# Optimization experiments

Hardware: AMD Instinct MI355X
Metric: run time of the kernel (lower is better)

The kernel has to match this reference:

```python
import jax, jax.numpy as jnp
import numpy as np

B, T, H, E = 256, 512, 512, 32

def setup_inputs() -> dict:
    key = jax.random.key(0)
    ks = jax.random.split(key, 7)
    events = jax.random.randint(ks[0], (B, T), 0, E, dtype=jnp.int32)
    # strictly increasing event times (as produced by cumsum of positive gaps upstream)
    gaps = jax.random.uniform(ks[1], (B, T), dtype=jnp.float32) * 0.1 + 1e-3
    times = jnp.cumsum(gaps, axis=1)
    emb = jax.random.normal(ks[2], (E, H), dtype=jnp.float32) * 0.05
    # 5 gate Linears (input, forget, output, cell, decay) stacked: [2H, 5H]
    W_gates = jax.random.normal(ks[3], (2 * H, 5 * H), dtype=jnp.float32) * (1.0 / np.sqrt(2 * H))
    b_gates = jnp.zeros((5 * H,), dtype=jnp.float32)
    W_int = jax.random.normal(ks[4], (H, E), dtype=jnp.float32) * (1.0 / np.sqrt(H))
    b_int = jnp.zeros((E,), dtype=jnp.float32)
    return {"events": events, "times": times, "emb": emb,
            "W_gates": W_gates, "b_gates": b_gates, "W_int": W_int, "b_int": b_int}

def reference(events, times, emb, W_gates, b_gates, W_int, b_int):
    Bs, Ts = events.shape
    Hs = emb.shape[1]
    x_seq = emb[events]                                   # [B,T,H] embedding lookup
    deltas = jnp.concatenate([times[:, :1], jnp.diff(times, axis=1)], axis=1)  # [B,T]
    xs = (jnp.transpose(x_seq, (1, 0, 2)), deltas.T)      # ([T,B,H], [T,B])

    def step(carry, inp):
        h, c = carry
        x, dt = inp
        comb = jnp.concatenate([x, h], axis=1)            # [B,2H]
        g = comb @ W_gates + b_gates                      # [B,5H] fused gate GEMM
        i, f, o, c_tilde, d = jnp.split(g, 5, axis=1)
        i, f, o, c_tilde = jnp.tanh(i), jnp.tanh(f), jnp.tanh(o), jnp.tanh(c_tilde)
        decay = jax.nn.softplus(d)
        c_dec = c * jnp.exp(-decay * dt[:, None])
        c_n = f * c_dec + i * c_tilde
        h_n = o * jnp.tanh(c_n)
        lam = jax.nn.softplus(h_n @ W_int + b_int)        # [B,E]
        return (h_n, c_n), (lam, h_n)

    h0 = jnp.zeros((Bs, Hs), dtype=times.dtype)
    c0 = jnp.zeros((Bs, Hs), dtype=times.dtype)
    _, (lams, hs) = jax.lax.scan(step, (h0, c0), xs)
    intensities = jnp.transpose(lams, (1, 0, 2))          # [B,T,E]
    hidden_states = jnp.transpose(hs, (1, 0, 2))          # [B,T,H]
    return intensities, hidden_states
```

## Files before the change

kernel.cpp:

```cpp
#include <hip/hip_runtime.h>
#include <math.h>


#define Bb   256
#define Tt   512
#define Hh   512
#define Ee   32
#define G5H  2560
#define NTHR 256
#define RT   16
#define CT   32

typedef __attribute__((ext_vector_type(8))) short f16x8;
typedef __attribute__((ext_vector_type(4))) float f32x4;
typedef __attribute__((ext_vector_type(4))) unsigned u32x4;
typedef __attribute__((ext_vector_type(2))) unsigned u32x2;

__device__ __forceinline__ float softplusf(float x) {
    return fmaxf(x, 0.f) + __logf(1.f + __expf(-fabsf(x)));
}
__device__ __forceinline__ float fast_tanh(float x) {
    const float t = fminf(fmaxf(x, -15.f), 15.f);
    const float e = __expf(2.f * t);
    return (e - 1.f) / (e + 1.f);
}
__device__ __forceinline__ unsigned short f2h(float f) {
    _Float16 h = (_Float16)f;
    return *reinterpret_cast<unsigned short*>(&h);
}

__device__ __forceinline__ void load_tagged8(const unsigned* p, u32x4 (&d)[8]) {
    asm volatile(
        "global_load_dwordx4 %0, %8, off sc0 sc1\n\t"
        "global_load_dwordx4 %1, %8, off offset:16 sc0 sc1\n\t"
        "global_load_dwordx4 %2, %8, off offset:128 sc0 sc1\n\t"
        "global_load_dwordx4 %3, %8, off offset:144 sc0 sc1\n\t"
        "global_load_dwordx4 %4, %8, off offset:256 sc0 sc1\n\t"
        "global_load_dwordx4 %5, %8, off offset:272 sc0 sc1\n\t"
        "global_load_dwordx4 %6, %8, off offset:384 sc0 sc1\n\t"
        "global_load_dwordx4 %7, %8, off offset:400 sc0 sc1\n\t"
        "s_waitcnt vmcnt(0)"
        : "=&v"(d[0]), "=&v"(d[1]), "=&v"(d[2]), "=&v"(d[3]),
          "=&v"(d[4]), "=&v"(d[5]), "=&v"(d[6]), "=&v"(d[7])
        : "v"(p) : "memory");
}
__device__ __forceinline__ void store_tagged(unsigned* p, unsigned data, unsigned tag) {
    u32x2 v; v.x = data; v.y = tag;
    asm volatile("global_store_dwordx2 %0, %1, off sc0 sc1"
                 :: "v"(p), "v"(v) : "memory");
}

__global__ __launch_bounds__(NTHR, 1)
void nhp_scan(const int* __restrict__ events, const float* __restrict__ times,
              const float* __restrict__ emb, const float* __restrict__ Wg,
              const float* __restrict__ bg, float* __restrict__ out_hid,
              unsigned* __restrict__ hb) {
    __shared__ float red[2][4][10][16][18];
    __shared__ float gx[Ee][5][34];
    __shared__ int   ev_s[2][RT];
    __shared__ float dt_s[2][RT];

    const int tid  = threadIdx.x, bid = blockIdx.x;
    const int rt   = bid & 15;
    const int ct   = bid >> 4;
    const int r0   = rt * RT;
    const int lane = tid & 63;
    const int ks   = tid >> 6;
    const int frow = lane & 15, kgrp = lane >> 4;
    const int erow = tid >> 4;
    const int ecp  = (tid & 15) * 2;

    for (int u = tid; u < Ee * 5 * CT; u += NTHR) {
        const int e = u / 160, r = u - e * 160;
        const int g = r >> 5, hc = r & 31;
        const int gcol = g * Hh + ct * CT + hc;
        float acc = bg[gcol];
        const float* er = emb + (size_t)e * Hh;
        for (int k = 0; k < Hh; k += 4) {
            acc += er[k]     * Wg[(size_t)k       * G5H + gcol];
            acc += er[k + 1] * Wg[(size_t)(k + 1) * G5H + gcol];
            acc += er[k + 2] * Wg[(size_t)(k + 2) * G5H + gcol];
            acc += er[k + 3] * Wg[(size_t)(k + 3) * G5H + gcol];
        }
        gx[e][g][hc ^ ((e & 7) << 2)] = acc;
    }

    f16x8 Bf[10][4];
    #pragma unroll
    for (int n = 0; n < 10; ++n) {
        const int col = (n >> 1) * Hh + ct * CT + (n & 1) * 16 + frow;
        #pragma unroll
        for (int kk = 0; kk < 4; ++kk) {
            const int k0 = ks * 128 + kk * 32 + kgrp * 8;
            union { f16x8 v; unsigned u[4]; } tmp;
            #pragma unroll
            for (int r = 0; r < 4; ++r) {
                const float w0 = Wg[(size_t)(Hh + k0 + 2 * r)     * G5H + col];
                const float w1 = Wg[(size_t)(Hh + k0 + 2 * r + 1) * G5H + col];
                tmp.u[r] = (unsigned)f2h(w0) | ((unsigned)f2h(w1) << 16);
            }
            Bf[n][kk] = tmp.v;
        }
    }

    float cA = 0.f, cB = 0.f;
    __syncthreads();

    for (int p = 0; p < Tt; ++p) {
        const int par = p & 1;
        if (tid < RT) {
            const int b = r0 + tid;
            ev_s[par][tid] = events[b * Tt + p];
            const float tp = times[b * Tt + p];
            dt_s[par][tid] = (p == 0) ? tp : tp - times[b * Tt + p - 1];
        }

        if (p > 0) {
            const unsigned* base = hb + ((size_t)((p - 1) & 1) * Bb * 256
                                 + (size_t)(r0 + frow) * 256 + ks * 64 + kgrp * 4) * 2;
            const unsigned want = (unsigned)p;
            u32x4 d[8];
            int guard = 0;
            for (;;) {
                load_tagged8(base, d);
                int ok = 1;
                #pragma unroll
                for (int i = 0; i < 8; ++i)
                    ok &= (d[i].y == want) & (d[i].w == want);
                if (__all(ok)) break;
                if (++guard > 100000) break;
                __builtin_amdgcn_s_sleep(1);
            }
            f16x8 a[4];
            #pragma unroll
            for (int kk = 0; kk < 4; ++kk) {
                union { f16x8 v; unsigned u[4]; } t;
                t.u[0] = d[2 * kk].x;     t.u[1] = d[2 * kk].z;
                t.u[2] = d[2 * kk + 1].x; t.u[3] = d[2 * kk + 1].z;
                a[kk] = t.v;
            }
            f32x4 acc[10];
            #pragma unroll
            for (int n = 0; n < 10; ++n) acc[n] = (f32x4){0.f, 0.f, 0.f, 0.f};
            #pragma unroll
            for (int kk = 0; kk < 4; ++kk) {
                #pragma unroll
                for (int n = 0; n < 10; ++n)
                    acc[n] = __builtin_amdgcn_mfma_f32_16x16x32_f16(
                        a[kk], Bf[n][kk], acc[n], 0, 0, 0);
            }
            #pragma unroll
            for (int n = 0; n < 10; ++n)
                #pragma unroll
                for (int r = 0; r < 4; ++r)
                    red[par][ks][n][kgrp * 4 + r][frow] = acc[n][r];
        }
        __syncthreads();

        const int   e  = ev_s[par][erow];
        const float dt = dt_s[par][erow];
        const int   sc = (e & 7) << 2;
        float hn[2];
        {
            float v0[5], v1[5];
            const int tl0 = ecp >> 4, fc = ecp & 15;
            #pragma unroll
            for (int gt = 0; gt < 5; ++gt) {
                const float2 gv = *(const float2*)&gx[e][gt][ecp ^ sc];
                v0[gt] = gv.x; v1[gt] = gv.y;
                if (p > 0) {
                    const int tl = gt * 2 + tl0;
                    #pragma unroll
                    for (int s = 0; s < 4; ++s) {
                        const float2 pr = *(const float2*)&red[par][s][tl][erow][fc];
                        v0[gt] += pr.x; v1[gt] += pr.y;
                    }
                }
            }
            #pragma unroll
            for (int q = 0; q < 2; ++q) {
                const float* v = q ? v1 : v0;
                const float ig  = fast_tanh(v[0]);
                const float fg  = fast_tanh(v[1]);
                const float og  = fast_tanh(v[2]);
                const float ctl = fast_tanh(v[3]);
                const float dec = softplusf(v[4]);
                const float cpv = q ? cB : cA;
                const float cn  = fg * (cpv * __expf(-dec * dt)) + ig * ctl;
                if (q) cB = cn; else cA = cn;
                hn[q] = og * fast_tanh(cn);
            }
        }

        const unsigned pk = (unsigned)f2h(hn[0]) | ((unsigned)f2h(hn[1]) << 16);
        store_tagged(hb + ((size_t)par * Bb * 256 + (size_t)(r0 + erow) * 256
                           + ct * 16 + (ecp >> 1)) * 2, pk, (unsigned)(p + 1));

        float2 ho; ho.x = hn[0]; ho.y = hn[1];
        *(float2*)(out_hid + ((size_t)(r0 + erow) * Tt + p) * Hh + ct * CT + ecp) = ho;
    }
}

__global__ __launch_bounds__(NTHR)
void nhp_intens(const float* __restrict__ out_hid, const float* __restrict__ Wi,
                const float* __restrict__ bi, float* __restrict__ out_int) {
    const int tid  = threadIdx.x;
    const int w    = tid >> 6;
    const int lane = tid & 63;
    const int col  = lane & 15, kgrp = lane >> 4;

    f16x8 Bfi[2][16];
    #pragma unroll
    for (int n = 0; n < 2; ++n)
        #pragma unroll
        for (int kk = 0; kk < 16; ++kk) {
            const int k0 = kk * 32 + kgrp * 8;
            union { f16x8 v; unsigned u[4]; } tmp;
            #pragma unroll
            for (int r = 0; r < 4; ++r) {
                const float w0 = Wi[(size_t)(k0 + 2 * r)     * Ee + n * 16 + col];
                const float w1 = Wi[(size_t)(k0 + 2 * r + 1) * Ee + n * 16 + col];
                tmp.u[r] = (unsigned)f2h(w0) | ((unsigned)f2h(w1) << 16);
            }
            Bfi[n][kk] = tmp.v;
        }
    const float bv[2] = { bi[col], bi[16 + col] };

    #pragma unroll
    for (int it = 0; it < 2; ++it) {
        const size_t rowbase = (size_t)blockIdx.x * 128 + (w * 2 + it) * 16;
        f32x4 acc0 = (f32x4){0.f,0.f,0.f,0.f}, acc1 = acc0;
        #pragma unroll
        for (int kk = 0; kk < 16; ++kk) {
            const float* hp = out_hid + (rowbase + (lane & 15)) * Hh + kk * 32 + kgrp * 8;
            const float4 hA = *(const float4*)hp;
            const float4 hB = *(const float4*)(hp + 4);
            union { f16x8 v; unsigned u[4]; } t;
            t.u[0] = (unsigned)f2h(hA.x) | ((unsigned)f2h(hA.y) << 16);
            t.u[1] = (unsigned)f2h(hA.z) | ((unsigned)f2h(hA.w) << 16);
            t.u[2] = (unsigned)f2h(hB.x) | ((unsigned)f2h(hB.y) << 16);
            t.u[3] = (unsigned)f2h(hB.z) | ((unsigned)f2h(hB.w) << 16);
            acc0 = __builtin_amdgcn_mfma_f32_16x16x32_f16(t.v, Bfi[0][kk], acc0, 0, 0, 0);
            acc1 = __builtin_amdgcn_mfma_f32_16x16x32_f16(t.v, Bfi[1][kk], acc1, 0, 0, 0);
        }
        #pragma unroll
        for (int i = 0; i < 4; ++i) {
            const size_t row = rowbase + kgrp * 4 + i;
            out_int[row * Ee + col]      = softplusf(acc0[i] + bv[0]);
            out_int[row * Ee + 16 + col] = softplusf(acc1[i] + bv[1]);
        }
    }
}

extern "C" void kernel_launch(void* const* d_in, const int* in_sizes, int n_in,
                              void* d_out, int out_size, void* d_ws, size_t ws_size,
                              hipStream_t stream) {
    const int*   events = (const int*)d_in[0];
    const float* times  = (const float*)d_in[1];
    const float* emb    = (const float*)d_in[2];
    const float* Wg     = (const float*)d_in[3];
    const float* bg     = (const float*)d_in[4];
    const float* Wi     = (const float*)d_in[5];
    const float* bi     = (const float*)d_in[6];
    float* out_int = (float*)d_out;
    float* out_hid = out_int + (size_t)Bb * Tt * Ee;
    unsigned* hb = (unsigned*)d_ws;

    hipMemsetAsync(hb, 0, 2u * Bb * 256 * 8, stream);
    hipLaunchKernelGGL(nhp_scan, dim3(256), dim3(NTHR), 0, stream,
                       events, times, emb, Wg, bg, out_hid, hb);
    hipLaunchKernelGGL(nhp_intens, dim3((Bb * Tt) / 128), dim3(NTHR), 0, stream,
                       out_hid, Wi, bi, out_int);
}
```

Baseline: 2.469 ms.

## Add fast-path cross-block handoff with weaker cache scope and generation tags

```diff
diff --git a/kernel.cpp b/kernel.cpp
--- a/kernel.cpp
+++ b/kernel.cpp
@@ -29,7 +29,7 @@
     return *reinterpret_cast<unsigned short*>(&h);
 }
 
-__device__ __forceinline__ void load_tagged8(const unsigned* p, u32x4 (&d)[8]) {
+__device__ __forceinline__ void load_slow8(const unsigned* p, u32x4 (&d)[8]) {
     asm volatile(
         "global_load_dwordx4 %0, %8, off sc0 sc1\n\t"
         "global_load_dwordx4 %1, %8, off offset:16 sc0 sc1\n\t"
@@ -44,21 +44,57 @@
           "=&v"(d[4]), "=&v"(d[5]), "=&v"(d[6]), "=&v"(d[7])
         : "v"(p) : "memory");
 }
-__device__ __forceinline__ void store_tagged(unsigned* p, unsigned data, unsigned tag) {
+__device__ __forceinline__ void load_fast8(const unsigned* p, u32x4 (&d)[8]) {
+    asm volatile(
+        "global_load_dwordx4 %0, %8, off sc0\n\t"
+        "global_load_dwordx4 %1, %8, off offset:16 sc0\n\t"
+        "global_load_dwordx4 %2, %8, off offset:128 sc0\n\t"
+        "global_load_dwordx4 %3, %8, off offset:144 sc0\n\t"
+        "global_load_dwordx4 %4, %8, off offset:256 sc0\n\t"
+        "global_load_dwordx4 %5, %8, off offset:272 sc0\n\t"
+        "global_load_dwordx4 %6, %8, off offset:384 sc0\n\t"
+        "global_load_dwordx4 %7, %8, off offset:400 sc0\n\t"
+        "s_waitcnt vmcnt(0)"
+        : "=&v"(d[0]), "=&v"(d[1]), "=&v"(d[2]), "=&v"(d[3]),
+          "=&v"(d[4]), "=&v"(d[5]), "=&v"(d[6]), "=&v"(d[7])
+        : "v"(p) : "memory");
+}
+__device__ __forceinline__ void st_tag_slow(unsigned* p, unsigned data, unsigned tag) {
     u32x2 v; v.x = data; v.y = tag;
     asm volatile("global_store_dwordx2 %0, %1, off sc0 sc1"
                  :: "v"(p), "v"(v) : "memory");
+}
+__device__ __forceinline__ void st_tag_fast(unsigned* p, unsigned data, unsigned tag) {
+    u32x2 v; v.x = data; v.y = tag;
+    asm volatile("global_store_dwordx2 %0, %1, off"
+                 :: "v"(p), "v"(v) : "memory");
+}
+__device__ __forceinline__ unsigned ld_u32_slow(const unsigned* p) {
+    unsigned v;
+    asm volatile("global_load_dword %0, %1, off sc0 sc1\n\ts_waitcnt vmcnt(0)"
+                 : "=v"(v) : "v"(p) : "memory");
+    return v;
+}
+
+__global__ void nhp_gen(unsigned* __restrict__ slot) {
+    if (threadIdx.x == 0) {
+        unsigned g = ld_u32_slow(slot) + 1u;
+        asm volatile("global_store_dword %0, %1, off sc0 sc1"
+                     :: "v"(slot), "v"(g) : "memory");
+    }
 }
 
 __global__ __launch_bounds__(NTHR, 1)
 void nhp_scan(const int* __restrict__ events, const float* __restrict__ times,
               const float* __restrict__ emb, const float* __restrict__ Wg,
               const float* __restrict__ bg, float* __restrict__ out_hid,
-              unsigned* __restrict__ hb) {
+              const unsigned* __restrict__ gen_slot,
+              unsigned* __restrict__ hbs, unsigned* __restrict__ hbf) {
     __shared__ float red[2][4][10][16][18];
     __shared__ float gx[Ee][5][34];
     __shared__ int   ev_s[2][RT];
     __shared__ float dt_s[2][RT];
+    __shared__ unsigned gen_s;
 
     const int tid  = threadIdx.x, bid = blockIdx.x;
     const int rt   = bid & 15;
@@ -69,6 +105,8 @@
     const int frow = lane & 15, kgrp = lane >> 4;
     const int erow = tid >> 4;
     const int ecp  = (tid & 15) * 2;
+
+    if (tid == 0) gen_s = ld_u32_slow(gen_slot);
 
     for (int u = tid; u < Ee * 5 * CT; u += NTHR) {
         const int e = u / 160, r = u - e * 160;
@@ -105,6 +143,8 @@
 
     float cA = 0.f, cB = 0.f;
     __syncthreads();
+    const unsigned gen = gen_s;
+    int fastN = 40;
 
     for (int p = 0; p < Tt; ++p) {
         const int par = p & 1;
@@ -116,21 +156,35 @@
         }
 
         if (p > 0) {
-            const unsigned* base = hb + ((size_t)((p - 1) & 1) * Bb * 256
-                                 + (size_t)(r0 + frow) * 256 + ks * 64 + kgrp * 4) * 2;
-            const unsigned want = (unsigned)p;
+            const size_t off = ((size_t)((p - 1) & 1) * Bb * 256
+                             + (size_t)(r0 + frow) * 256 + ks * 64 + kgrp * 4) * 2;
             u32x4 d[8];
-            int guard = 0;
-            for (;;) {
-                load_tagged8(base, d);
+            const unsigned want_f = (gen << 10) | (unsigned)p;
+            int got = 0;
+            for (int t = 0; t < fastN; ++t) {
+                load_fast8(hbf + off, d);
                 int ok = 1;
                 #pragma unroll
                 for (int i = 0; i < 8; ++i)
-                    ok &= (d[i].y == want) & (d[i].w == want);
-                if (__all(ok)) break;
-                if (++guard > 100000) break;
+                    ok &= (d[i].y == want_f) & (d[i].w == want_f);
+                if (__all(ok)) { got = 1; break; }
                 __builtin_amdgcn_s_sleep(1);
             }
+            if (!got) {
+                const unsigned want_s = (unsigned)p;
+                int guard = 0;
+                for (;;) {
+                    load_slow8(hbs + off, d);
+                    int ok = 1;
+                    #pragma unroll
+                    for (int i = 0; i < 8; ++i)
+                        ok &= (d[i].y == want_s) & (d[i].w == want_s);
+                    if (__all(ok)) break;
+                    if (++guard > 100000) break;
+                    __builtin_amdgcn_s_sleep(1);
+                }
+                fastN = 2;
+            } else fastN = 40;
             f16x8 a[4];
             #pragma unroll
             for (int kk = 0; kk < 4; ++kk) {
@@ -193,8 +247,10 @@
         }
 
         const unsigned pk = (unsigned)f2h(hn[0]) | ((unsigned)f2h(hn[1]) << 16);
-        store_tagged(hb + ((size_t)par * Bb * 256 + (size_t)(r0 + erow) * 256
-                           + ct * 16 + (ecp >> 1)) * 2, pk, (unsigned)(p + 1));
+        const size_t uoff = ((size_t)par * Bb * 256 + (size_t)(r0 + erow) * 256
+                             + ct * 16 + (ecp >> 1)) * 2;
+        st_tag_fast(hbf + uoff, pk, (gen << 10) | (unsigned)(p + 1));
+        st_tag_slow(hbs + uoff, pk, (unsigned)(p + 1));
 
         float2 ho; ho.x = hn[0]; ho.y = hn[1];
         *(float2*)(out_hid + ((size_t)(r0 + erow) * Tt + p) * Hh + ct * CT + ecp) = ho;
@@ -264,11 +320,15 @@
     const float* bi     = (const float*)d_in[6];
     float* out_int = (float*)d_out;
     float* out_hid = out_int + (size_t)Bb * Tt * Ee;
-    unsigned* hb = (unsigned*)d_ws;
-
-    hipMemsetAsync(hb, 0, 2u * Bb * 256 * 8, stream);
+    const size_t HBSZ = (size_t)2 * Bb * 256 * 8;
+    unsigned* gen  = (unsigned*)d_ws;
+    unsigned* hbs  = (unsigned*)((char*)d_ws + 4096);
+    unsigned* hbf  = (unsigned*)((char*)d_ws + 4096 + HBSZ);
+
+    hipMemsetAsync((char*)d_ws + 4096, 0, 2 * HBSZ, stream);
+    hipLaunchKernelGGL(nhp_gen, dim3(1), dim3(64), 0, stream, gen);
     hipLaunchKernelGGL(nhp_scan, dim3(256), dim3(NTHR), 0, stream,
-                       events, times, emb, Wg, bg, out_hid, hb);
+                       events, times, emb, Wg, bg, out_hid, gen, hbs, hbf);
     hipLaunchKernelGGL(nhp_intens, dim3((Bb * Tt) / 128), dim3(NTHR), 0, stream,
                        out_hid, Wi, bi, out_int);
 }
```

Result: slower. 8.462 ms (+242.7%).

## Preload events and deltas to LDS, defer hidden-state store past spin wait

Applied to the files above, without the earlier changes.

```diff
diff --git a/kernel.cpp b/kernel.cpp
--- a/kernel.cpp
+++ b/kernel.cpp
@@ -29,7 +29,7 @@
     return *reinterpret_cast<unsigned short*>(&h);
 }
 
-__device__ __forceinline__ void load_tagged8(const unsigned* p, u32x4 (&d)[8]) {
+__device__ __forceinline__ void load_slow8(const unsigned* p, u32x4 (&d)[8]) {
     asm volatile(
         "global_load_dwordx4 %0, %8, off sc0 sc1\n\t"
         "global_load_dwordx4 %1, %8, off offset:16 sc0 sc1\n\t"
@@ -44,7 +44,7 @@
           "=&v"(d[4]), "=&v"(d[5]), "=&v"(d[6]), "=&v"(d[7])
         : "v"(p) : "memory");
 }
-__device__ __forceinline__ void store_tagged(unsigned* p, unsigned data, unsigned tag) {
+__device__ __forceinline__ void st_tag(unsigned* p, unsigned data, unsigned tag) {
     u32x2 v; v.x = data; v.y = tag;
     asm volatile("global_store_dwordx2 %0, %1, off sc0 sc1"
                  :: "v"(p), "v"(v) : "memory");
@@ -54,11 +54,11 @@
 void nhp_scan(const int* __restrict__ events, const float* __restrict__ times,
               const float* __restrict__ emb, const float* __restrict__ Wg,
               const float* __restrict__ bg, float* __restrict__ out_hid,
-              unsigned* __restrict__ hb) {
-    __shared__ float red[2][4][10][16][18];
+              unsigned* __restrict__ hbs) {
+    __shared__ float red[4][10][16][18];
     __shared__ float gx[Ee][5][34];
-    __shared__ int   ev_s[2][RT];
-    __shared__ float dt_s[2][RT];
+    __shared__ float dt_lds[RT][516];
+    __shared__ unsigned char ev_lds[RT][520];
 
     const int tid  = threadIdx.x, bid = blockIdx.x;
     const int rt   = bid & 15;
@@ -69,6 +69,14 @@
     const int frow = lane & 15, kgrp = lane >> 4;
     const int erow = tid >> 4;
     const int ecp  = (tid & 15) * 2;
+
+    for (int u = tid; u < RT * Tt; u += NTHR) {
+        const int row = u >> 9, pp = u & 511;
+        const float t1 = times[(r0 + row) * Tt + pp];
+        const float t0 = pp ? times[(r0 + row) * Tt + pp - 1] : 0.f;
+        dt_lds[row][pp] = t1 - t0;
+        ev_lds[row][pp] = (unsigned char)events[(r0 + row) * Tt + pp];
+    }
 
     for (int u = tid; u < Ee * 5 * CT; u += NTHR) {
         const int e = u / 160, r = u - e * 160;
@@ -104,25 +112,18 @@
     }
 
     float cA = 0.f, cB = 0.f;
+    float2 prev_hn;
     __syncthreads();
 
     for (int p = 0; p < Tt; ++p) {
-        const int par = p & 1;
-        if (tid < RT) {
-            const int b = r0 + tid;
-            ev_s[par][tid] = events[b * Tt + p];
-            const float tp = times[b * Tt + p];
-            dt_s[par][tid] = (p == 0) ? tp : tp - times[b * Tt + p - 1];
-        }
-
         if (p > 0) {
-            const unsigned* base = hb + ((size_t)((p - 1) & 1) * Bb * 256
-                                 + (size_t)(r0 + frow) * 256 + ks * 64 + kgrp * 4) * 2;
+            const size_t off = ((size_t)((p - 1) & 1) * Bb * 256
+                             + (size_t)(r0 + frow) * 256 + ks * 64 + kgrp * 4) * 2;
             const unsigned want = (unsigned)p;
             u32x4 d[8];
             int guard = 0;
             for (;;) {
-                load_tagged8(base, d);
+                load_slow8(hbs + off, d);
                 int ok = 1;
                 #pragma unroll
                 for (int i = 0; i < 8; ++i)
@@ -131,6 +132,10 @@
                 if (++guard > 100000) break;
                 __builtin_amdgcn_s_sleep(1);
             }
+
+            *(float2*)(out_hid + ((size_t)(r0 + erow) * Tt + (p - 1)) * Hh
+                       + ct * CT + ecp) = prev_hn;
+
             f16x8 a[4];
             #pragma unroll
             for (int kk = 0; kk < 4; ++kk) {
@@ -149,16 +154,17 @@
                     acc[n] = __builtin_amdgcn_mfma_f32_16x16x32_f16(
                         a[kk], Bf[n][kk], acc[n], 0, 0, 0);
             }
+            __syncthreads();
             #pragma unroll
             for (int n = 0; n < 10; ++n)
                 #pragma unroll
                 for (int r = 0; r < 4; ++r)
-                    red[par][ks][n][kgrp * 4 + r][frow] = acc[n][r];
-        }
-        __syncthreads();
-
-        const int   e  = ev_s[par][erow];
-        const float dt = dt_s[par][erow];
+                    red[ks][n][kgrp * 4 + r][frow] = acc[n][r];
+            __syncthreads();
+        }
+
+        const int   e  = ev_lds[erow][p];
+        const float dt = dt_lds[erow][p];
         const int   sc = (e & 7) << 2;
         float hn[2];
         {
@@ -172,7 +178,7 @@
                     const int tl = gt * 2 + tl0;
                     #pragma unroll
                     for (int s = 0; s < 4; ++s) {
-                        const float2 pr = *(const float2*)&red[par][s][tl][erow][fc];
+                        const float2 pr = *(const float2*)&red[s][tl][erow][fc];
                         v0[gt] += pr.x; v1[gt] += pr.y;
                     }
                 }
@@ -193,12 +199,13 @@
         }
 
         const unsigned pk = (unsigned)f2h(hn[0]) | ((unsigned)f2h(hn[1]) << 16);
-        store_tagged(hb + ((size_t)par * Bb * 256 + (size_t)(r0 + erow) * 256
-                           + ct * 16 + (ecp >> 1)) * 2, pk, (unsigned)(p + 1));
-
-        float2 ho; ho.x = hn[0]; ho.y = hn[1];
-        *(float2*)(out_hid + ((size_t)(r0 + erow) * Tt + p) * Hh + ct * CT + ecp) = ho;
-    }
+        st_tag(hbs + ((size_t)(p & 1) * Bb * 256 + (size_t)(r0 + erow) * 256
+                      + ct * 16 + (ecp >> 1)) * 2, pk, (unsigned)(p + 1));
+
+        prev_hn.x = hn[0]; prev_hn.y = hn[1];
+    }
+    *(float2*)(out_hid + ((size_t)(r0 + erow) * Tt + (Tt - 1)) * Hh
+               + ct * CT + ecp) = prev_hn;
 }
 
 __global__ __launch_bounds__(NTHR)
@@ -264,11 +271,11 @@
     const float* bi     = (const float*)d_in[6];
     float* out_int = (float*)d_out;
     float* out_hid = out_int + (size_t)Bb * Tt * Ee;
-    unsigned* hb = (unsigned*)d_ws;
-
-    hipMemsetAsync(hb, 0, 2u * Bb * 256 * 8, stream);
+    unsigned* hbs = (unsigned*)((char*)d_ws + 4096);
+
+    hipMemsetAsync(hbs, 0, (size_t)2 * Bb * 256 * 8, stream);
     hipLaunchKernelGGL(nhp_scan, dim3(256), dim3(NTHR), 0, stream,
-                       events, times, emb, Wg, bg, out_hid, hb);
+                       events, times, emb, Wg, bg, out_hid, hbs);
     hipLaunchKernelGGL(nhp_intens, dim3((Bb * Tt) / 128), dim3(NTHR), 0, stream,
                        out_hid, Wi, bi, out_int);
 }
```

New measurement: 2.505 ms. No clear change (+1.5%).
